# Performance work log

Measured on AMD Instinct MI355X. Metric: run time of the kernel, lower is better.

Reference implementation:

```python
import jax, jax.numpy as jnp
from jax import lax
import numpy as np

V, D, H = 50257, 128, 256  # vocab, d_model, d_hidden
B, T = 16, 128             # batch, seq_len


def setup_inputs() -> dict:
    key = jax.random.key(0)
    k_ids, k_emb, k_wih, k_whh, k_out = jax.random.split(key, 5)
    s = 0.02
    return {
        "input_ids": jax.random.randint(k_ids, (B, T), 0, V, dtype=jnp.int64 if jax.config.jax_enable_x64 else jnp.int32),
        "embed": jax.random.normal(k_emb, (V, D), jnp.float32) * s,
        "W_ih": jax.random.normal(k_wih, (3 * H, D), jnp.float32) * s,
        "b_ih": jnp.zeros((3 * H,), jnp.float32),
        "W_hh": jax.random.normal(k_whh, (3 * H, H), jnp.float32) * s,
        "b_hh": jnp.zeros((3 * H,), jnp.float32),
        "W_out": jax.random.normal(k_out, (V, H), jnp.float32) * s,
    }


def reference(input_ids, embed, W_ih, b_ih, W_hh, b_hh, W_out):
    # Embedding lookup: [B,T,D]
    x = embed[input_ids]
    # Precompute input-side gate projections for all timesteps: [B,T,3H]
    gx_all = jnp.einsum('btd,gd->btg', x, W_ih) + b_ih

    def step(h, gx):
        # h: [B,H], gx: [B,3H]
        gh = h @ W_hh.T + b_hh  # [B,3H]
        xr, xz, xn = jnp.split(gx, 3, axis=-1)
        hr, hz, hn = jnp.split(gh, 3, axis=-1)
        r = jax.nn.sigmoid(xr + hr)
        z = jax.nn.sigmoid(xz + hz)
        n = jnp.tanh(xn + r * hn)  # PyTorch GRU: r gates the hidden projection
        h_new = (1.0 - z) * n + z * h
        return h_new, h_new

    h0 = jnp.zeros((x.shape[0], W_hh.shape[1]), x.dtype)
    _, hs = lax.scan(step, h0, jnp.swapaxes(gx_all, 0, 1))  # hs: [T,B,H]
    out = jnp.swapaxes(hs, 0, 1)  # [B,T,H]
    # LM head (no bias): [B,T,V]
    return jnp.einsum('bth,vh->btv', out, W_out)
```

## Files before the change

### kernel.cpp

```cpp
#include <hip/hip_runtime.h>
#include <hip/hip_bf16.h>

#define V    50257
#define VPAD 50304
#define DD   128
#define HH   256
#define G3   768
#define BB   16
#define TT   128

typedef _Float16 h2   __attribute__((ext_vector_type(2)));
typedef _Float16 h8   __attribute__((ext_vector_type(8)));
typedef short  bf16x8 __attribute__((ext_vector_type(8)));
typedef float  f32x4  __attribute__((ext_vector_type(4)));

typedef __attribute__((address_space(3))) uint4* lds_u4_t;
typedef const __attribute__((address_space(1))) uint4* gbl_u4_t;

__device__ __forceinline__ void async_copy16(const uint4* g, uint4* lds_base) {
    __builtin_amdgcn_global_load_lds((gbl_u4_t)g, (lds_u4_t)lds_base, 16, 0, 0);
}

#if __has_builtin(__builtin_amdgcn_fdot2)
#define USE_FDOT2 1
#else
#define USE_FDOT2 0
#endif

__device__ __forceinline__ float sigmoid_(float x) { return 1.0f / (1.0f + __expf(-x)); }
__device__ __forceinline__ float tanh_(float x)    { float e = __expf(2.0f * x); return (e - 1.0f) / (e + 1.0f); }

__global__ __launch_bounds__(256) void k_embed_gx(
    const int* __restrict__ ids, const float* __restrict__ embed,
    const float* __restrict__ W_ih, const float* __restrict__ b_ih,
    float* __restrict__ gx)
{
    __shared__ float xs[8][DD];
    const int tid  = threadIdx.x;
    const int row0 = blockIdx.x * 8;

#pragma unroll
    for (int i = 0; i < 4; ++i) {
        int e = tid + i * 256;
        int r = e >> 7, k = e & 127;
        int id = ids[row0 + r];
        xs[r][k] = embed[(long)id * DD + k];
    }
    __syncthreads();

#pragma unroll
    for (int o = 0; o < 3; ++o) {
        int j = tid + o * 256;
        float bias = b_ih[j];
        float acc[8];
#pragma unroll
        for (int r = 0; r < 8; ++r) acc[r] = bias;
        const float4* wrow = (const float4*)(W_ih + (long)j * DD);
        for (int q = 0; q < 32; ++q) {
            float4 w = wrow[q];
#pragma unroll
            for (int r = 0; r < 8; ++r) {
                acc[r] += w.x * xs[r][q * 4 + 0] + w.y * xs[r][q * 4 + 1]
                        + w.z * xs[r][q * 4 + 2] + w.w * xs[r][q * 4 + 3];
            }
        }
#pragma unroll
        for (int r = 0; r < 8; ++r) gx[(long)(row0 + r) * G3 + j] = acc[r];
    }
}

__global__ __launch_bounds__(256) void k_convert_wout(
    const float* __restrict__ Wout, __hip_bfloat16* __restrict__ Wb)
{
    long base = ((long)blockIdx.x * 256 + threadIdx.x) * 8;
    const long VALID = (long)V * HH;
    union { __hip_bfloat16 b[8]; uint4 u; } pk;
    if (base < VALID) {
        float4 f0 = ((const float4*)Wout)[base / 4];
        float4 f1 = ((const float4*)Wout)[base / 4 + 1];
        pk.b[0] = __float2bfloat16(f0.x); pk.b[1] = __float2bfloat16(f0.y);
        pk.b[2] = __float2bfloat16(f0.z); pk.b[3] = __float2bfloat16(f0.w);
        pk.b[4] = __float2bfloat16(f1.x); pk.b[5] = __float2bfloat16(f1.y);
        pk.b[6] = __float2bfloat16(f1.z); pk.b[7] = __float2bfloat16(f1.w);
    } else {
        pk.u = make_uint4(0, 0, 0, 0);
    }
    *(uint4*)(Wb + base) = pk.u;
}

__global__ __launch_bounds__(512, 2) void k_gru(
    const float* __restrict__ gx, const float* __restrict__ W_hh,
    const float* __restrict__ b_hh, __hip_bfloat16* __restrict__ hout)
{
    __shared__ _Float16 hh[2][HH];
    const int tid = threadIdx.x;
    const int b   = blockIdx.x;
    const int g   = tid >> 1;
    const int u   = tid & 1;

    h2 w[3][64];
#pragma unroll
    for (int o = 0; o < 3; ++o) {
        const float4* wr = (const float4*)(W_hh + (long)(o * 256 + g) * HH + u * 128);
#pragma unroll
        for (int q = 0; q < 32; ++q) {
            float4 f = wr[q];
            w[o][2 * q]     = h2{(_Float16)f.x, (_Float16)f.y};
            w[o][2 * q + 1] = h2{(_Float16)f.z, (_Float16)f.w};
        }
    }
    float bias[3];
#pragma unroll
    for (int o = 0; o < 3; ++o) bias[o] = b_hh[o * 256 + g];

    if (tid < HH) hh[0][tid] = (_Float16)0.0f;
    __syncthreads();

    const float* gxrow = gx + (long)b * TT * G3;
    float cxr = gxrow[g], cxz = gxrow[256 + g], cxn = gxrow[512 + g];
    float hold = 0.0f;

    for (int t = 0; t < TT; ++t) {
        const float* nrow = gxrow + G3;
        float nxr = nrow[g], nxz = nrow[256 + g], nxn = nrow[512 + g];

        float a0a = 0.f, a0b = 0.f, a1a = 0.f, a1b = 0.f, a2a = 0.f, a2b = 0.f;
        const h8* hp8 = ((const h8*)hh[t & 1]) + u * 16;
#pragma unroll
        for (int c = 0; c < 16; ++c) {
            h8 hv = hp8[c];
            const h2* hvp = (const h2*)&hv;
#pragma unroll
            for (int j = 0; j < 4; ++j) {
                h2 hq = hvp[j];
                int p = c * 4 + j;
#if USE_FDOT2
                if (j & 1) {
                    a0b = __builtin_amdgcn_fdot2(w[0][p], hq, a0b, false);
                    a1b = __builtin_amdgcn_fdot2(w[1][p], hq, a1b, false);
                    a2b = __builtin_amdgcn_fdot2(w[2][p], hq, a2b, false);
                } else {
                    a0a = __builtin_amdgcn_fdot2(w[0][p], hq, a0a, false);
                    a1a = __builtin_amdgcn_fdot2(w[1][p], hq, a1a, false);
                    a2a = __builtin_amdgcn_fdot2(w[2][p], hq, a2a, false);
                }
#else
                float hx = (float)hq.x, hy = (float)hq.y;
                if (j & 1) {
                    a0b += (float)w[0][p].x * hx + (float)w[0][p].y * hy;
                    a1b += (float)w[1][p].x * hx + (float)w[1][p].y * hy;
                    a2b += (float)w[2][p].x * hx + (float)w[2][p].y * hy;
                } else {
                    a0a += (float)w[0][p].x * hx + (float)w[0][p].y * hy;
                    a1a += (float)w[1][p].x * hx + (float)w[1][p].y * hy;
                    a2a += (float)w[2][p].x * hx + (float)w[2][p].y * hy;
                }
#endif
            }
        }
        float acc0 = a0a + a0b, acc1 = a1a + a1b, acc2 = a2a + a2b;
        acc0 += __shfl_xor(acc0, 1);
        acc1 += __shfl_xor(acc1, 1);
        acc2 += __shfl_xor(acc2, 1);

        float r = sigmoid_(cxr + acc0 + bias[0]);
        float z = sigmoid_(cxz + acc1 + bias[1]);
        float n = tanh_(cxn + r * (acc2 + bias[2]));
        float hnew = (1.0f - z) * n + z * hold;

        if (u == 0) hh[(t + 1) & 1][g] = (_Float16)hnew;
        else        hout[((long)b * TT + t) * HH + g] = __float2bfloat16(hnew);
        __syncthreads();

        hold = hnew;
        cxr = nxr; cxz = nxz; cxn = nxn;
        gxrow = nrow;
    }
}

__global__ __launch_bounds__(256) void k_head(
    const __hip_bfloat16* __restrict__ Ah, const __hip_bfloat16* __restrict__ Bw,
    float* __restrict__ out)
{
    __shared__ unsigned short As[128 * 64];
    __shared__ unsigned short Bs[128 * 64];
    const int i    = threadIdx.x;
    const int wave = i >> 6, lane = i & 63;
    const int quad = lane >> 4, mr = lane & 15;
    const int m0   = blockIdx.y * 128;
    const int n0   = blockIdx.x * 128;
    const int wm0  = (wave >> 1) * 64;
    const int wn0  = (wave & 1) * 64;

    f32x4 acc[4][4];
#pragma unroll
    for (int a = 0; a < 4; ++a)
#pragma unroll
        for (int c = 0; c < 4; ++c) acc[a][c] = (f32x4){0.f, 0.f, 0.f, 0.f};

    const uint4* Ag = (const uint4*)Ah;
    const uint4* Bg = (const uint4*)Bw;
    uint4* Asv = (uint4*)As;
    uint4* Bsv = (uint4*)Bs;

    const uint4* agp[4]; const uint4* bgp[4];
    uint4* alds[4]; uint4* blds[4];
#pragma unroll
    for (int c = 0; c < 4; ++c) {
        int seg   = c * 4 + wave;
        int row   = seg * 8 + (lane >> 3);
        int chunk = (lane & 7) ^ (row & 7);
        agp[c] = Ag + (long)(m0 + row) * 32 + chunk;
        bgp[c] = Bg + (long)(n0 + row) * 32 + chunk;
        alds[c] = Asv + seg * 64;
        blds[c] = Bsv + seg * 64;
    }

    for (int ks = 0; ks < 4; ++ks) {
        __syncthreads();
#pragma unroll
        for (int c = 0; c < 4; ++c) async_copy16(agp[c] + ks * 8, alds[c]);
#pragma unroll
        for (int c = 0; c < 4; ++c) async_copy16(bgp[c] + ks * 8, blds[c]);
        __syncthreads();

#pragma unroll
        for (int kk = 0; kk < 2; ++kk) {
            bf16x8 af[4], bf[4];
#pragma unroll
            for (int wmi = 0; wmi < 4; ++wmi) {
                int row  = wm0 + wmi * 16 + mr;
                int slot = (kk * 4 + quad) ^ (row & 7);
                af[wmi] = *(const bf16x8*)&As[(row * 8 + slot) * 8];
            }
#pragma unroll
            for (int wni = 0; wni < 4; ++wni) {
                int row  = wn0 + wni * 16 + mr;
                int slot = (kk * 4 + quad) ^ (row & 7);
                bf[wni] = *(const bf16x8*)&Bs[(row * 8 + slot) * 8];
            }
#pragma unroll
            for (int wmi = 0; wmi < 4; ++wmi)
#pragma unroll
                for (int wni = 0; wni < 4; ++wni)
                    acc[wmi][wni] = __builtin_amdgcn_mfma_f32_16x16x32_bf16(
                        af[wmi], bf[wni], acc[wmi][wni], 0, 0, 0);
        }
    }

#pragma unroll
    for (int wmi = 0; wmi < 4; ++wmi) {
#pragma unroll
        for (int rr = 0; rr < 4; ++rr) {
            long m = m0 + wm0 + wmi * 16 + quad * 4 + rr;
            float* orow = out + m * (long)V;
#pragma unroll
            for (int wni = 0; wni < 4; ++wni) {
                int n = n0 + wn0 + wni * 16 + mr;
                if (n < V) orow[n] = acc[wmi][wni][rr];
            }
        }
    }
}

extern "C" void kernel_launch(void* const* d_in, const int* in_sizes, int n_in,
                              void* d_out, int out_size, void* d_ws, size_t ws_size,
                              hipStream_t stream) {
    const int*   ids   = (const int*)d_in[0];
    const float* embed = (const float*)d_in[1];
    const float* W_ih  = (const float*)d_in[2];
    const float* b_ih  = (const float*)d_in[3];
    const float* W_hh  = (const float*)d_in[4];
    const float* b_hh  = (const float*)d_in[5];
    const float* W_out = (const float*)d_in[6];
    float* out = (float*)d_out;

    char* ws = (char*)d_ws;
    float*          gx  = (float*)ws;
    __hip_bfloat16* hbf = (__hip_bfloat16*)(ws + 6291456);
    __hip_bfloat16* wbf = (__hip_bfloat16*)(ws + 7340032);

    k_embed_gx<<<256, 256, 0, stream>>>(ids, embed, W_ih, b_ih, gx);
    k_convert_wout<<<6288, 256, 0, stream>>>(W_out, wbf);
    k_gru<<<16, 512, 0, stream>>>(gx, W_hh, b_hh, hbf);
    k_head<<<dim3(393, 16), 256, 0, stream>>>(hbf, wbf, out);
}
```

Before: 770.3 us.

## Overlap W_out conversion with GRU recurrence and retile LM head GEMM

Merges the W_out bf16 conversion into the GRU launch as extra blocks, so the conversion runs on idle CUs while the 16 serial GRU blocks execute, and one launch is removed. The GRU inner loop now batches four LDS loads ahead of the dot products. The LM head GEMM is retiled to 512x64 tiles with 8 waves, each covering 64 rows, so the A tile is reused across more rows and fewer blocks are launched. The larger LDS footprint and the waves_per_eu constraint may limit occupancy, and conversion blocks could compete with the GRU blocks for CU resources.

```diff
diff --git a/kernel.cpp b/kernel.cpp
--- a/kernel.cpp
+++ b/kernel.cpp
@@ -30,7 +30,7 @@
 __device__ __forceinline__ float sigmoid_(float x) { return 1.0f / (1.0f + __expf(-x)); }
 __device__ __forceinline__ float tanh_(float x)    { float e = __expf(2.0f * x); return (e - 1.0f) / (e + 1.0f); }
 
-__global__ __launch_bounds__(256) void k_embed_gx(
+__global__ __launch_bounds__(256) void k_embed(
     const int* __restrict__ ids, const float* __restrict__ embed,
     const float* __restrict__ W_ih, const float* __restrict__ b_ih,
     float* __restrict__ gx)
@@ -69,34 +69,37 @@
     }
 }
 
-__global__ __launch_bounds__(256) void k_convert_wout(
+__global__ __launch_bounds__(512)
+__attribute__((amdgpu_waves_per_eu(2, 2)))
+void k_gruconv(
+    const float* __restrict__ gx, const float* __restrict__ W_hh,
+    const float* __restrict__ b_hh, __hip_bfloat16* __restrict__ hout,
     const float* __restrict__ Wout, __hip_bfloat16* __restrict__ Wb)
 {
-    long base = ((long)blockIdx.x * 256 + threadIdx.x) * 8;
-    const long VALID = (long)V * HH;
-    union { __hip_bfloat16 b[8]; uint4 u; } pk;
-    if (base < VALID) {
-        float4 f0 = ((const float4*)Wout)[base / 4];
-        float4 f1 = ((const float4*)Wout)[base / 4 + 1];
-        pk.b[0] = __float2bfloat16(f0.x); pk.b[1] = __float2bfloat16(f0.y);
-        pk.b[2] = __float2bfloat16(f0.z); pk.b[3] = __float2bfloat16(f0.w);
-        pk.b[4] = __float2bfloat16(f1.x); pk.b[5] = __float2bfloat16(f1.y);
-        pk.b[6] = __float2bfloat16(f1.z); pk.b[7] = __float2bfloat16(f1.w);
-    } else {
-        pk.u = make_uint4(0, 0, 0, 0);
-    }
-    *(uint4*)(Wb + base) = pk.u;
-}
-
-__global__ __launch_bounds__(512, 2) void k_gru(
-    const float* __restrict__ gx, const float* __restrict__ W_hh,
-    const float* __restrict__ b_hh, __hip_bfloat16* __restrict__ hout)
-{
+    const int tid = threadIdx.x;
+
+    if (blockIdx.x >= 16) {
+        long base = ((long)(blockIdx.x - 16) * 512 + tid) * 8;
+        const long VALID = (long)V * HH;
+        union { __hip_bfloat16 b[8]; uint4 u; } pk;
+        if (base < VALID) {
+            float4 f0 = ((const float4*)Wout)[base / 4];
+            float4 f1 = ((const float4*)Wout)[base / 4 + 1];
+            pk.b[0] = __float2bfloat16(f0.x); pk.b[1] = __float2bfloat16(f0.y);
+            pk.b[2] = __float2bfloat16(f0.z); pk.b[3] = __float2bfloat16(f0.w);
+            pk.b[4] = __float2bfloat16(f1.x); pk.b[5] = __float2bfloat16(f1.y);
+            pk.b[6] = __float2bfloat16(f1.z); pk.b[7] = __float2bfloat16(f1.w);
+        } else {
+            pk.u = make_uint4(0, 0, 0, 0);
+        }
+        *(uint4*)(Wb + base) = pk.u;
+        return;
+    }
+
     __shared__ _Float16 hh[2][HH];
-    const int tid = threadIdx.x;
-    const int b   = blockIdx.x;
-    const int g   = tid >> 1;
-    const int u   = tid & 1;
+    const int b = blockIdx.x;
+    const int g = tid >> 1;
+    const int u = tid & 1;
 
     h2 w[3][64];
 #pragma unroll
@@ -127,35 +130,43 @@
         float a0a = 0.f, a0b = 0.f, a1a = 0.f, a1b = 0.f, a2a = 0.f, a2b = 0.f;
         const h8* hp8 = ((const h8*)hh[t & 1]) + u * 16;
 #pragma unroll
-        for (int c = 0; c < 16; ++c) {
-            h8 hv = hp8[c];
-            const h2* hvp = (const h2*)&hv;
-#pragma unroll
-            for (int j = 0; j < 4; ++j) {
-                h2 hq = hvp[j];
-                int p = c * 4 + j;
+        for (int cc = 0; cc < 4; ++cc) {
+            h8 hv0 = hp8[cc * 4 + 0];
+            h8 hv1 = hp8[cc * 4 + 1];
+            h8 hv2 = hp8[cc * 4 + 2];
+            h8 hv3 = hp8[cc * 4 + 3];
+            asm volatile("" ::: "memory");
+            const h8 hvs[4] = {hv0, hv1, hv2, hv3};
+#pragma unroll
+            for (int c2 = 0; c2 < 4; ++c2) {
+                const h2* hvp = (const h2*)&hvs[c2];
+#pragma unroll
+                for (int j = 0; j < 4; ++j) {
+                    h2 hq = hvp[j];
+                    int p = (cc * 4 + c2) * 4 + j;
 #if USE_FDOT2
-                if (j & 1) {
-                    a0b = __builtin_amdgcn_fdot2(w[0][p], hq, a0b, false);
-                    a1b = __builtin_amdgcn_fdot2(w[1][p], hq, a1b, false);
-                    a2b = __builtin_amdgcn_fdot2(w[2][p], hq, a2b, false);
-                } else {
-                    a0a = __builtin_amdgcn_fdot2(w[0][p], hq, a0a, false);
-                    a1a = __builtin_amdgcn_fdot2(w[1][p], hq, a1a, false);
-                    a2a = __builtin_amdgcn_fdot2(w[2][p], hq, a2a, false);
+                    if (j & 1) {
+                        a0b = __builtin_amdgcn_fdot2(w[0][p], hq, a0b, false);
+                        a1b = __builtin_amdgcn_fdot2(w[1][p], hq, a1b, false);
+                        a2b = __builtin_amdgcn_fdot2(w[2][p], hq, a2b, false);
+                    } else {
+                        a0a = __builtin_amdgcn_fdot2(w[0][p], hq, a0a, false);
+                        a1a = __builtin_amdgcn_fdot2(w[1][p], hq, a1a, false);
+                        a2a = __builtin_amdgcn_fdot2(w[2][p], hq, a2a, false);
+                    }
+#else
+                    float hx = (float)hq.x, hy = (float)hq.y;
+                    if (j & 1) {
+                        a0b += (float)w[0][p].x * hx + (float)w[0][p].y * hy;
+                        a1b += (float)w[1][p].x * hx + (float)w[1][p].y * hy;
+                        a2b += (float)w[2][p].x * hx + (float)w[2][p].y * hy;
+                    } else {
+                        a0a += (float)w[0][p].x * hx + (float)w[0][p].y * hy;
+                        a1a += (float)w[1][p].x * hx + (float)w[1][p].y * hy;
+                        a2a += (float)w[2][p].x * hx + (float)w[2][p].y * hy;
+                    }
+#endif
                 }
-#else
-                float hx = (float)hq.x, hy = (float)hq.y;
-                if (j & 1) {
-                    a0b += (float)w[0][p].x * hx + (float)w[0][p].y * hy;
-                    a1b += (float)w[1][p].x * hx + (float)w[1][p].y * hy;
-                    a2b += (float)w[2][p].x * hx + (float)w[2][p].y * hy;
-                } else {
-                    a0a += (float)w[0][p].x * hx + (float)w[0][p].y * hy;
-                    a1a += (float)w[1][p].x * hx + (float)w[1][p].y * hy;
-                    a2a += (float)w[2][p].x * hx + (float)w[2][p].y * hy;
-                }
-#endif
             }
         }
         float acc0 = a0a + a0b, acc1 = a1a + a1b, acc2 = a2a + a2b;
@@ -178,19 +189,18 @@
     }
 }
 
-__global__ __launch_bounds__(256) void k_head(
+__global__ __launch_bounds__(512, 4) void k_head(
     const __hip_bfloat16* __restrict__ Ah, const __hip_bfloat16* __restrict__ Bw,
     float* __restrict__ out)
 {
-    __shared__ unsigned short As[128 * 64];
-    __shared__ unsigned short Bs[128 * 64];
+    __shared__ unsigned short As[512 * 64];
+    __shared__ unsigned short Bs[64 * 64];
     const int i    = threadIdx.x;
     const int wave = i >> 6, lane = i & 63;
     const int quad = lane >> 4, mr = lane & 15;
-    const int m0   = blockIdx.y * 128;
-    const int n0   = blockIdx.x * 128;
-    const int wm0  = (wave >> 1) * 64;
-    const int wn0  = (wave & 1) * 64;
+    const int m0   = blockIdx.y * 512;
+    const int n0   = blockIdx.x * 64;
+    const int wm0  = wave * 64;
 
     f32x4 acc[4][4];
 #pragma unroll
@@ -203,40 +213,31 @@
     uint4* Asv = (uint4*)As;
     uint4* Bsv = (uint4*)Bs;
 
-    const uint4* agp[4]; const uint4* bgp[4];
-    uint4* alds[4]; uint4* blds[4];
-#pragma unroll
-    for (int c = 0; c < 4; ++c) {
-        int seg   = c * 4 + wave;
-        int row   = seg * 8 + (lane >> 3);
-        int chunk = (lane & 7) ^ (row & 7);
-        agp[c] = Ag + (long)(m0 + row) * 32 + chunk;
-        bgp[c] = Bg + (long)(n0 + row) * 32 + chunk;
-        alds[c] = Asv + seg * 64;
-        blds[c] = Bsv + seg * 64;
-    }
+    const int lrow = lane >> 3;
+    const int lchk = (lane & 7) ^ lrow;
+    const uint4* aBase = Ag + (long)(m0 + wave * 8 + lrow) * 32 + lchk;
+    const uint4* bBase = Bg + (long)(n0 + wave * 8 + lrow) * 32 + lchk;
 
     for (int ks = 0; ks < 4; ++ks) {
         __syncthreads();
 #pragma unroll
-        for (int c = 0; c < 4; ++c) async_copy16(agp[c] + ks * 8, alds[c]);
-#pragma unroll
-        for (int c = 0; c < 4; ++c) async_copy16(bgp[c] + ks * 8, blds[c]);
+        for (int c = 0; c < 8; ++c)
+            async_copy16(aBase + (long)c * 2048 + ks * 8, Asv + (c * 8 + wave) * 64);
+        async_copy16(bBase + ks * 8, Bsv + wave * 64);
         __syncthreads();
 
 #pragma unroll
         for (int kk = 0; kk < 2; ++kk) {
+            const int slot = (kk * 4 + quad) ^ (mr & 7);
             bf16x8 af[4], bf[4];
 #pragma unroll
             for (int wmi = 0; wmi < 4; ++wmi) {
-                int row  = wm0 + wmi * 16 + mr;
-                int slot = (kk * 4 + quad) ^ (row & 7);
+                int row = wm0 + wmi * 16 + mr;
                 af[wmi] = *(const bf16x8*)&As[(row * 8 + slot) * 8];
             }
 #pragma unroll
             for (int wni = 0; wni < 4; ++wni) {
-                int row  = wn0 + wni * 16 + mr;
-                int slot = (kk * 4 + quad) ^ (row & 7);
+                int row = wni * 16 + mr;
                 bf[wni] = *(const bf16x8*)&Bs[(row * 8 + slot) * 8];
             }
 #pragma unroll
@@ -256,7 +257,7 @@
             float* orow = out + m * (long)V;
 #pragma unroll
             for (int wni = 0; wni < 4; ++wni) {
-                int n = n0 + wn0 + wni * 16 + mr;
+                int n = n0 + wni * 16 + mr;
                 if (n < V) orow[n] = acc[wmi][wni][rr];
             }
         }
@@ -280,8 +281,7 @@
     __hip_bfloat16* hbf = (__hip_bfloat16*)(ws + 6291456);
     __hip_bfloat16* wbf = (__hip_bfloat16*)(ws + 7340032);
 
-    k_embed_gx<<<256, 256, 0, stream>>>(ids, embed, W_ih, b_ih, gx);
-    k_convert_wout<<<6288, 256, 0, stream>>>(W_out, wbf);
-    k_gru<<<16, 512, 0, stream>>>(gx, W_hh, b_hh, hbf);
-    k_head<<<dim3(393, 16), 256, 0, stream>>>(hbf, wbf, out);
-}
+    k_embed<<<256, 256, 0, stream>>>(ids, embed, W_ih, b_ih, gx);
+    k_gruconv<<<3160, 512, 0, stream>>>(gx, W_hh, b_hh, hbf, W_out, wbf);
+    k_head<<<dim3(786, 4), 512, 0, stream>>>(hbf, wbf, out);
+}
```

New measurement: 786.3 us. 1.02x slower.
